# Optimization experiments

Measured on AMD Instinct MI355X. Metric: run time of the kernel, lower is better.

Reference implementation:

```python
import jax, jax.numpy as jnp
import numpy as np


def setup_inputs() -> dict:
    key = jax.random.key(0)
    k1, k2, k3 = jax.random.split(key, 3)
    N, C, W = 32, 64, 4096
    F, WW = 128, 64
    x = jax.random.normal(k1, (N, C, W), dtype=jnp.float32)
    w = jax.random.normal(k2, (F, C, WW), dtype=jnp.float32)
    b = jax.random.normal(k3, (F,), dtype=jnp.float32)
    return {"x": x, "w": w, "b": b}


def reference(x, w, b):
    # FFT-based 1D cross-correlation (the original loops over N, F, C; here batched).
    # x: [N, C, W], w: [F, C, WW], b: [F]
    N, C, W = x.shape
    F, _, WW = w.shape
    pad = 0  # module's padding kwarg
    fftsize = 1 << int(np.ceil(np.log2(W + 2 * pad + WW - 1)))  # next_power2
    out_W = W + 2 * pad - WW + 1
    # rfft of zero-padded signals and filters
    xfft = jnp.fft.rfft(x, n=fftsize, axis=-1)          # [N, C, K]
    wfft = jnp.fft.rfft(w, n=fftsize, axis=-1)          # [F, C, K]
    # cross-correlation: multiply by conj of filter spectrum, sum over channels
    offt = jnp.einsum('nck,fck->nfk', xfft, jnp.conj(wfft))  # [N, F, K]
    out = jnp.fft.irfft(offt, n=fftsize, axis=-1)[..., :out_W]  # real part, first out_W samples
    return out + b[None, :, None]
```

## Files before the change

### kernel.cpp

```cpp
#include <hip/hip_runtime.h>


#define C_TOT   64
#define F_TOT   128
#define KW      64
#define OUT_W   4033
#define W_IN    4096
#define N_BATCH 32
#define T_BLK   256
#define CH      2
#define XWIN    320
#define XSTR    384
#define TRS     260

typedef __attribute__((ext_vector_type(8))) short  short8;
typedef __attribute__((ext_vector_type(4))) float  floatx4;

union Frag { unsigned int u[4]; short8 v; };

__device__ inline unsigned short f32_to_bf16(float f) {
  unsigned int u = __float_as_uint(f);
  u += 0x7FFF + ((u >> 16) & 1);
  return (unsigned short)(u >> 16);
}

__device__ inline void async16(const unsigned short* g, unsigned short* l) {
  __builtin_amdgcn_global_load_lds(
      (const __attribute__((address_space(1))) unsigned int*)g,
      (__attribute__((address_space(3))) unsigned int*)l, 16, 0, 0);
}

__global__ __launch_bounds__(256) void conv1d_prep(
    const float* __restrict__ w, unsigned short* __restrict__ wsw) {
  int i4 = blockIdx.x * 256 + threadIdx.x;
  if (i4 < F_TOT * C_TOT * KW / 4) {
    int k4 = (i4 & 15) * 4;
    int c  = (i4 >> 4) & 63;
    int f  = i4 >> 10;
    float4 v = *(const float4*)&w[(size_t)i4 * 4];
    ushort4 o;
    o.x = f32_to_bf16(v.x); o.y = f32_to_bf16(v.y);
    o.z = f32_to_bf16(v.z); o.w = f32_to_bf16(v.w);
    int chunk = (k4 >> 3) ^ (f & 7);
    *(ushort4*)&wsw[((size_t)(c * F_TOT + f) * 8 + chunk) * 8 + (k4 & 7)] = o;
  }
}

__global__ __launch_bounds__(256, 2) void conv1d_mfma(
    const float* __restrict__ x, const unsigned short* __restrict__ wsw,
    const float* __restrict__ b, float* __restrict__ out) {
  __shared__ union SM {
    struct {
      unsigned short wls[2][CH * F_TOT * KW];
      unsigned short xls[2][CH * XSTR];
    } k;
    float tr[32 * TRS];
  } sm;

  const int tid  = threadIdx.x;
  const int lane = tid & 63;
  const int wv   = tid >> 6;
  const int q    = lane >> 4;
  const int col  = lane & 15;
  const int n    = blockIdx.y;
  const int t0   = blockIdx.x * T_BLK;
  const int fh2  = wv & 1;
  const int th   = wv >> 1;

  const int xc = tid / 80;
  const int xi = (tid - xc * 80) * 4;
  const float* xrowb = x + (size_t)n * C_TOT * W_IN;

  floatx4 acc[8][4];
#pragma unroll
  for (int ms = 0; ms < 8; ++ms)
#pragma unroll
    for (int ft = 0; ft < 4; ++ft) acc[ms][ft] = (floatx4)0.0f;

#define LOAD_X(cgx, vv)                                                         \
  {                                                                             \
    const float* src = xrowb + (size_t)((cgx) * CH + xc) * W_IN;                \
    int gt = t0 + xi;                                                           \
    if (gt + 3 < W_IN) vv = *(const float4*)(src + gt);                         \
    else {                                                                      \
      if (gt < W_IN)     vv.x = src[gt];                                        \
      if (gt + 1 < W_IN) vv.y = src[gt + 1];                                    \
      if (gt + 2 < W_IN) vv.z = src[gt + 2];                                    \
    }                                                                           \
  }

#define WRITE_X(p, vv)                                                          \
  {                                                                             \
    ushort4 o;                                                                  \
    o.x = f32_to_bf16(vv.x); o.y = f32_to_bf16(vv.y);                           \
    o.z = f32_to_bf16(vv.z); o.w = f32_to_bf16(vv.w);                           \
    *(ushort4*)&sm.k.xls[p][xc * XSTR + xi] = o;                                \
  }

#define STAGE_W(cg, p)                                                          \
  {                                                                             \
    const unsigned short* wbase = wsw + (size_t)(cg) * (CH * F_TOT * KW);       \
    _Pragma("unroll")                                                           \
    for (int s = 0; s < 8; ++s) {                                               \
      int off = (wv * 8 + s) * 512;                                             \
      async16(wbase + off + lane * 8, &sm.k.wls[p][off]);                       \
    }                                                                           \
  }

  if (tid < 160) {
    float4 xv = {0.f, 0.f, 0.f, 0.f};
    LOAD_X(0, xv)
    WRITE_X(0, xv)
  }
  STAGE_W(0, 0)
  __syncthreads();

  for (int cg = 0; cg < C_TOT / CH; ++cg) {
    const int p = cg & 1;
    const bool pre = (cg < C_TOT / CH - 1);
    float4 xv = {0.f, 0.f, 0.f, 0.f};
    if (pre && tid < 160) LOAD_X(cg + 1, xv)
    if (pre) STAGE_W(cg + 1, p ^ 1)

#pragma unroll
    for (int chl = 0; chl < CH; ++chl) {
      const unsigned short* xpb = &sm.k.xls[p][chl * XSTR];
      const unsigned short* wpb = &sm.k.wls[p][chl * F_TOT * KW];
#pragma unroll
      for (int h = 0; h < 2; ++h) {
        const int ab = 16 * col + 256 * th + 64 * h + 16 * q;
        const uint4 d0 = *(const uint4*)((const char*)xpb + ab);
        const uint4 d1 = *(const uint4*)((const char*)xpb + ab + 16);
        const unsigned int D[8] = {d0.x, d0.y, d0.z, d0.w, d1.x, d1.y, d1.z, d1.w};
        Frag A[8];
#pragma unroll
        for (int s = 0; s < 4; ++s)
#pragma unroll
          for (int i = 0; i < 4; ++i) {
            A[2 * s].u[i]     = D[s + i];
            A[2 * s + 1].u[i] = (D[s + i] >> 16) | (D[s + i + 1] << 16);
          }
        const int bs = ((h * 4 + q) ^ (col & 7)) * 8;
#pragma unroll
        for (int ft = 0; ft < 4; ++ft) {
          const short8 bf =
              *(const short8*)&wpb[(fh2 * 64 + ft * 16 + col) * KW + bs];
#pragma unroll
          for (int ms = 0; ms < 8; ++ms)
            acc[ms][ft] =
                __builtin_amdgcn_mfma_f32_16x16x32_bf16(A[ms].v, bf, acc[ms][ft], 0, 0, 0);
        }
      }
    }
    if (pre && tid < 160) WRITE_X(p ^ 1, xv)
    __syncthreads();
  }

  const int fs_w  = fh2 * 16 + col;
  const int fs_r  = tid >> 3;
  const int seg   = tid & 7;
  const int f_r   = (fs_r >> 4) * 64 + (fs_r & 15);
  const size_t ob = ((size_t)n * F_TOT) * OUT_W;

#pragma unroll
  for (int j = 0; j < 4; ++j) {
#pragma unroll
    for (int r = 0; r < 4; ++r)
#pragma unroll
      for (int g = 0; g < 2; ++g) {
        float4 vv;
        vv.x = acc[g * 4 + 0][j][r];
        vv.y = acc[g * 4 + 1][j][r];
        vv.z = acc[g * 4 + 2][j][r];
        vv.w = acc[g * 4 + 3][j][r];
        int tl = 32 * q + 8 * r + 4 * g + 128 * th;
        *(float4*)&sm.tr[fs_w * TRS + tl] = vv;
      }
    __syncthreads();
    const int f = f_r + 16 * j;
    const float bias = b[f];
    const size_t obf = ob + (size_t)f * OUT_W;
#pragma unroll
    for (int j2 = 0; j2 < 8; ++j2) {
      int tl = seg * 4 + 32 * j2;
      float4 vv = *(const float4*)&sm.tr[fs_r * TRS + tl];
      vv.x += bias; vv.y += bias; vv.z += bias; vv.w += bias;
      int t = t0 + tl;
      if (t + 3 < OUT_W) {
        *(float4*)&out[obf + t] = vv;
      } else {
        float e[4] = {vv.x, vv.y, vv.z, vv.w};
#pragma unroll
        for (int u = 0; u < 4; ++u)
          if (t + u < OUT_W) out[obf + t + u] = e[u];
      }
    }
    __syncthreads();
  }
}

extern "C" void kernel_launch(void* const* d_in, const int* in_sizes, int n_in,
                              void* d_out, int out_size, void* d_ws, size_t ws_size,
                              hipStream_t stream) {
  const float* x = (const float*)d_in[0];
  const float* w = (const float*)d_in[1];
  const float* b = (const float*)d_in[2];
  float* out = (float*)d_out;

  unsigned short* wsw = (unsigned short*)d_ws;

  conv1d_prep<<<(F_TOT * C_TOT * KW / 4 + 255) / 256, 256, 0, stream>>>(w, wsw);

  dim3 grid((OUT_W + T_BLK - 1) / T_BLK, N_BATCH);
  conv1d_mfma<<<grid, 256, 0, stream>>>(x, wsw, b, out);
}
```

Baseline: 186.2 us.

## Split filters across blocks to halve per-block tile and raise occupancy

Each block now computes 64 filters instead of 128, so the grid doubles to 32x32 blocks. This halves the accumulator registers and the weight LDS buffer, and launch bounds move to 4 blocks per SM. The MFMA inner loop is restructured to build A fragments per step rather than holding all eight. In exchange, each x tile is staged and converted twice, once for each filter half.

```diff
diff --git a/kernel.cpp b/kernel.cpp
--- a/kernel.cpp
+++ b/kernel.cpp
@@ -3,6 +3,7 @@
 
 #define C_TOT   64
 #define F_TOT   128
+#define F_BLK   64
 #define KW      64
 #define OUT_W   4033
 #define W_IN    4096
@@ -46,12 +47,12 @@
   }
 }
 
-__global__ __launch_bounds__(256, 2) void conv1d_mfma(
+__global__ __launch_bounds__(256, 4) void conv1d_mfma(
     const float* __restrict__ x, const unsigned short* __restrict__ wsw,
     const float* __restrict__ b, float* __restrict__ out) {
   __shared__ union SM {
     struct {
-      unsigned short wls[2][CH * F_TOT * KW];
+      unsigned short wls[2][CH * F_BLK * KW];
       unsigned short xls[2][CH * XSTR];
     } k;
     float tr[32 * TRS];
@@ -63,19 +64,21 @@
   const int q    = lane >> 4;
   const int col  = lane & 15;
   const int n    = blockIdx.y;
-  const int t0   = blockIdx.x * T_BLK;
-  const int fh2  = wv & 1;
+  const int bx   = blockIdx.x;
+  const int t0   = (bx & 15) * T_BLK;
+  const int FB   = (bx >> 4) * F_BLK;
+  const int fq   = wv & 1;
   const int th   = wv >> 1;
 
   const int xc = tid / 80;
   const int xi = (tid - xc * 80) * 4;
   const float* xrowb = x + (size_t)n * C_TOT * W_IN;
 
-  floatx4 acc[8][4];
+  floatx4 acc[8][2];
 #pragma unroll
   for (int ms = 0; ms < 8; ++ms)
 #pragma unroll
-    for (int ft = 0; ft < 4; ++ft) acc[ms][ft] = (floatx4)0.0f;
+    for (int ft = 0; ft < 2; ++ft) acc[ms][ft] = (floatx4)0.0f;
 
 #define LOAD_X(cgx, vv)                                                         \
   {                                                                             \
@@ -97,13 +100,15 @@
     *(ushort4*)&sm.k.xls[p][xc * XSTR + xi] = o;                                \
   }
 
-#define STAGE_W(cg, p)                                                          \
+#define STAGE_W(cg_, p_)                                                        \
   {                                                                             \
-    const unsigned short* wbase = wsw + (size_t)(cg) * (CH * F_TOT * KW);       \
+    const unsigned short* wb = wsw + ((size_t)(cg_) * CH * F_TOT + FB) * KW;    \
     _Pragma("unroll")                                                           \
-    for (int s = 0; s < 8; ++s) {                                               \
-      int off = (wv * 8 + s) * 512;                                             \
-      async16(wbase + off + lane * 8, &sm.k.wls[p][off]);                       \
+    for (int s = 0; s < 4; ++s) {                                               \
+      int off = (wv * 4 + s) * 512 + lane * 8;                                  \
+      int chl = off >> 12;                                                      \
+      int rem = off & 4095;                                                     \
+      async16(wb + (size_t)chl * F_TOT * KW + rem, &sm.k.wls[p_][off]);         \
     }                                                                           \
   }
 
@@ -125,30 +130,32 @@
 #pragma unroll
     for (int chl = 0; chl < CH; ++chl) {
       const unsigned short* xpb = &sm.k.xls[p][chl * XSTR];
-      const unsigned short* wpb = &sm.k.wls[p][chl * F_TOT * KW];
+      const unsigned short* wpb = &sm.k.wls[p][chl * F_BLK * KW];
 #pragma unroll
       for (int h = 0; h < 2; ++h) {
         const int ab = 16 * col + 256 * th + 64 * h + 16 * q;
         const uint4 d0 = *(const uint4*)((const char*)xpb + ab);
         const uint4 d1 = *(const uint4*)((const char*)xpb + ab + 16);
         const unsigned int D[8] = {d0.x, d0.y, d0.z, d0.w, d1.x, d1.y, d1.z, d1.w};
-        Frag A[8];
-#pragma unroll
-        for (int s = 0; s < 4; ++s)
+        const int bs = ((h * 4 + q) ^ (col & 7)) * 8;
+        const short8 bf0 = *(const short8*)&wpb[(fq * 32 + col) * KW + bs];
+        const short8 bf1 = *(const short8*)&wpb[(fq * 32 + 16 + col) * KW + bs];
+#pragma unroll
+        for (int s = 0; s < 4; ++s) {
+          Frag Ae, Ao;
 #pragma unroll
           for (int i = 0; i < 4; ++i) {
-            A[2 * s].u[i]     = D[s + i];
-            A[2 * s + 1].u[i] = (D[s + i] >> 16) | (D[s + i + 1] << 16);
+            Ae.u[i] = D[s + i];
+            Ao.u[i] = (D[s + i] >> 16) | (D[s + i + 1] << 16);
           }
-        const int bs = ((h * 4 + q) ^ (col & 7)) * 8;
-#pragma unroll
-        for (int ft = 0; ft < 4; ++ft) {
-          const short8 bf =
-              *(const short8*)&wpb[(fh2 * 64 + ft * 16 + col) * KW + bs];
-#pragma unroll
-          for (int ms = 0; ms < 8; ++ms)
-            acc[ms][ft] =
-                __builtin_amdgcn_mfma_f32_16x16x32_bf16(A[ms].v, bf, acc[ms][ft], 0, 0, 0);
+          acc[2 * s][0] =
+              __builtin_amdgcn_mfma_f32_16x16x32_bf16(Ae.v, bf0, acc[2 * s][0], 0, 0, 0);
+          acc[2 * s][1] =
+              __builtin_amdgcn_mfma_f32_16x16x32_bf16(Ae.v, bf1, acc[2 * s][1], 0, 0, 0);
+          acc[2 * s + 1][0] =
+              __builtin_amdgcn_mfma_f32_16x16x32_bf16(Ao.v, bf0, acc[2 * s + 1][0], 0, 0, 0);
+          acc[2 * s + 1][1] =
+              __builtin_amdgcn_mfma_f32_16x16x32_bf16(Ao.v, bf1, acc[2 * s + 1][1], 0, 0, 0);
         }
       }
     }
@@ -156,14 +163,13 @@
     __syncthreads();
   }
 
-  const int fs_w  = fh2 * 16 + col;
+  const int fs_w  = fq * 16 + col;
   const int fs_r  = tid >> 3;
   const int seg   = tid & 7;
-  const int f_r   = (fs_r >> 4) * 64 + (fs_r & 15);
   const size_t ob = ((size_t)n * F_TOT) * OUT_W;
 
 #pragma unroll
-  for (int j = 0; j < 4; ++j) {
+  for (int j = 0; j < 2; ++j) {
 #pragma unroll
     for (int r = 0; r < 4; ++r)
 #pragma unroll
@@ -177,7 +183,7 @@
         *(float4*)&sm.tr[fs_w * TRS + tl] = vv;
       }
     __syncthreads();
-    const int f = f_r + 16 * j;
+    const int f = FB + (fs_r >> 4) * 32 + j * 16 + (fs_r & 15);
     const float bias = b[f];
     const size_t obf = ob + (size_t)f * OUT_W;
 #pragma unroll
@@ -211,6 +217,6 @@
 
   conv1d_prep<<<(F_TOT * C_TOT * KW / 4 + 255) / 256, 256, 0, stream>>>(w, wsw);
 
-  dim3 grid((OUT_W + T_BLK - 1) / T_BLK, N_BATCH);
+  dim3 grid(32, N_BATCH);
   conv1d_mfma<<<grid, 256, 0, stream>>>(x, wsw, b, out);
 }
```

Result: slower. 225.5 us (+21.1%).

## Reorder conv GEMM reduction to iterate over taps with channel-major x tile

Applied to the files above, without the earlier changes.

The reduction loop changes from channel groups (reduce over the 64 filter taps inside each MFMA) to filter taps (reduce over channels inside each MFMA). The whole x window for all 64 channels is transposed into LDS once as bf16, and the weights are re-laid out per tap, so only a 16KB weight slice is streamed per step. This removes the register shuffling that built shifted A fragments and the per-iteration x loads. In exchange it adds a larger upfront x staging phase with scalar transposed LDS stores, and runs 64 barrier-synchronised iterations instead of 32.

```diff
diff --git a/kernel.cpp b/kernel.cpp
--- a/kernel.cpp
+++ b/kernel.cpp
@@ -8,15 +8,13 @@
 #define W_IN    4096
 #define N_BATCH 32
 #define T_BLK   256
-#define CH      2
-#define XWIN    320
-#define XSTR    384
+#define XROWS   320
+#define XSTR    72
 #define TRS     260
+#define BK_SH   8192
 
 typedef __attribute__((ext_vector_type(8))) short  short8;
 typedef __attribute__((ext_vector_type(4))) float  floatx4;
-
-union Frag { unsigned int u[4]; short8 v; };
 
 __device__ inline unsigned short f32_to_bf16(float f) {
   unsigned int u = __float_as_uint(f);
@@ -34,15 +32,17 @@
     const float* __restrict__ w, unsigned short* __restrict__ wsw) {
   int i4 = blockIdx.x * 256 + threadIdx.x;
   if (i4 < F_TOT * C_TOT * KW / 4) {
-    int k4 = (i4 & 15) * 4;
-    int c  = (i4 >> 4) & 63;
-    int f  = i4 >> 10;
-    float4 v = *(const float4*)&w[(size_t)i4 * 4];
+    int c4 = (i4 & 15) * 4;
+    int f  = (i4 >> 4) & 127;
+    int k  = i4 >> 11;
+    const float* src = w + ((size_t)f * C_TOT + c4) * KW + k;
     ushort4 o;
-    o.x = f32_to_bf16(v.x); o.y = f32_to_bf16(v.y);
-    o.z = f32_to_bf16(v.z); o.w = f32_to_bf16(v.w);
-    int chunk = (k4 >> 3) ^ (f & 7);
-    *(ushort4*)&wsw[((size_t)(c * F_TOT + f) * 8 + chunk) * 8 + (k4 & 7)] = o;
+    o.x = f32_to_bf16(src[0 * KW]);
+    o.y = f32_to_bf16(src[1 * KW]);
+    o.z = f32_to_bf16(src[2 * KW]);
+    o.w = f32_to_bf16(src[3 * KW]);
+    int chunk = (c4 >> 3) ^ (f & 7);
+    *(ushort4*)&wsw[((size_t)(k * F_TOT + f) * 8 + chunk) * 8 + (c4 & 7)] = o;
   }
 }
 
@@ -50,12 +50,10 @@
     const float* __restrict__ x, const unsigned short* __restrict__ wsw,
     const float* __restrict__ b, float* __restrict__ out) {
   __shared__ union SM {
-    struct {
-      unsigned short wls[2][CH * F_TOT * KW];
-      unsigned short xls[2][CH * XSTR];
-    } k;
+    unsigned short xt[XROWS * XSTR];
     float tr[32 * TRS];
   } sm;
+  __shared__ unsigned short bls[2][BK_SH];
 
   const int tid  = threadIdx.x;
   const int lane = tid & 63;
@@ -67,8 +65,6 @@
   const int fh2  = wv & 1;
   const int th   = wv >> 1;
 
-  const int xc = tid / 80;
-  const int xi = (tid - xc * 80) * 4;
   const float* xrowb = x + (size_t)n * C_TOT * W_IN;
 
   floatx4 acc[8][4];
@@ -77,82 +73,62 @@
 #pragma unroll
     for (int ft = 0; ft < 4; ++ft) acc[ms][ft] = (floatx4)0.0f;
 
-#define LOAD_X(cgx, vv)                                                         \
-  {                                                                             \
-    const float* src = xrowb + (size_t)((cgx) * CH + xc) * W_IN;                \
-    int gt = t0 + xi;                                                           \
-    if (gt + 3 < W_IN) vv = *(const float4*)(src + gt);                         \
-    else {                                                                      \
-      if (gt < W_IN)     vv.x = src[gt];                                        \
-      if (gt + 1 < W_IN) vv.y = src[gt + 1];                                    \
-      if (gt + 2 < W_IN) vv.z = src[gt + 2];                                    \
-    }                                                                           \
+#define STAGE_B(k_, p_)                                                        \
+  {                                                                            \
+    const unsigned short* wb = wsw + (size_t)(k_) * BK_SH;                     \
+    _Pragma("unroll")                                                          \
+    for (int s = 0; s < 4; ++s) {                                              \
+      int off = ((wv * 4 + s) * 64 + lane) * 8;                                \
+      async16(wb + off, &bls[p_][off]);                                        \
+    }                                                                          \
   }
 
-#define WRITE_X(p, vv)                                                          \
-  {                                                                             \
-    ushort4 o;                                                                  \
-    o.x = f32_to_bf16(vv.x); o.y = f32_to_bf16(vv.y);                           \
-    o.z = f32_to_bf16(vv.z); o.w = f32_to_bf16(vv.w);                           \
-    *(ushort4*)&sm.k.xls[p][xc * XSTR + xi] = o;                                \
+  STAGE_B(0, 0)
+#pragma unroll 4
+  for (int it = 0; it < 20; ++it) {
+    int j  = it * 256 + tid;
+    int c  = j / 80;
+    int tq = j - c * 80;
+    int gt = t0 + tq * 4;
+    const float* src = xrowb + (size_t)c * W_IN + gt;
+    float4 v = {0.f, 0.f, 0.f, 0.f};
+    if (gt + 3 < W_IN) v = *(const float4*)src;
+    else {
+      if (gt < W_IN)     v.x = src[0];
+      if (gt + 1 < W_IN) v.y = src[1];
+      if (gt + 2 < W_IN) v.z = src[2];
+    }
+    int rb = tq * 4;
+    sm.xt[(rb + 0) * XSTR + c] = f32_to_bf16(v.x);
+    sm.xt[(rb + 1) * XSTR + c] = f32_to_bf16(v.y);
+    sm.xt[(rb + 2) * XSTR + c] = f32_to_bf16(v.z);
+    sm.xt[(rb + 3) * XSTR + c] = f32_to_bf16(v.w);
   }
-
-#define STAGE_W(cg, p)                                                          \
-  {                                                                             \
-    const unsigned short* wbase = wsw + (size_t)(cg) * (CH * F_TOT * KW);       \
-    _Pragma("unroll")                                                           \
-    for (int s = 0; s < 8; ++s) {                                               \
-      int off = (wv * 8 + s) * 512;                                             \
-      async16(wbase + off + lane * 8, &sm.k.wls[p][off]);                       \
-    }                                                                           \
-  }
-
-  if (tid < 160) {
-    float4 xv = {0.f, 0.f, 0.f, 0.f};
-    LOAD_X(0, xv)
-    WRITE_X(0, xv)
-  }
-  STAGE_W(0, 0)
   __syncthreads();
 
-  for (int cg = 0; cg < C_TOT / CH; ++cg) {
-    const int p = cg & 1;
-    const bool pre = (cg < C_TOT / CH - 1);
-    float4 xv = {0.f, 0.f, 0.f, 0.f};
-    if (pre && tid < 160) LOAD_X(cg + 1, xv)
-    if (pre) STAGE_W(cg + 1, p ^ 1)
+#pragma unroll 2
+  for (int k = 0; k < KW; ++k) {
+    const int p = k & 1;
+    if (k + 1 < KW) STAGE_B(k + 1, p ^ 1)
+
+    const unsigned short* xk = &sm.xt[(th * 128 + col + k) * XSTR + q * 8];
+    const unsigned short* bp = &bls[p][(fh2 * 64 + col) * 64];
 
 #pragma unroll
-    for (int chl = 0; chl < CH; ++chl) {
-      const unsigned short* xpb = &sm.k.xls[p][chl * XSTR];
-      const unsigned short* wpb = &sm.k.wls[p][chl * F_TOT * KW];
+    for (int cstep = 0; cstep < 2; ++cstep) {
+      short8 Bf[4];
 #pragma unroll
-      for (int h = 0; h < 2; ++h) {
-        const int ab = 16 * col + 256 * th + 64 * h + 16 * q;
-        const uint4 d0 = *(const uint4*)((const char*)xpb + ab);
-        const uint4 d1 = *(const uint4*)((const char*)xpb + ab + 16);
-        const unsigned int D[8] = {d0.x, d0.y, d0.z, d0.w, d1.x, d1.y, d1.z, d1.w};
-        Frag A[8];
+      for (int ft = 0; ft < 4; ++ft)
+        Bf[ft] = *(const short8*)&bp[ft * 1024 + (((cstep << 2) + q) ^ (col & 7)) * 8];
 #pragma unroll
-        for (int s = 0; s < 4; ++s)
+      for (int ms = 0; ms < 8; ++ms) {
+        const short8 Af = *(const short8*)&xk[ms * 16 * XSTR + cstep * 32];
 #pragma unroll
-          for (int i = 0; i < 4; ++i) {
-            A[2 * s].u[i]     = D[s + i];
-            A[2 * s + 1].u[i] = (D[s + i] >> 16) | (D[s + i + 1] << 16);
-          }
-        const int bs = ((h * 4 + q) ^ (col & 7)) * 8;
-#pragma unroll
-        for (int ft = 0; ft < 4; ++ft) {
-          const short8 bf =
-              *(const short8*)&wpb[(fh2 * 64 + ft * 16 + col) * KW + bs];
-#pragma unroll
-          for (int ms = 0; ms < 8; ++ms)
-            acc[ms][ft] =
-                __builtin_amdgcn_mfma_f32_16x16x32_bf16(A[ms].v, bf, acc[ms][ft], 0, 0, 0);
-        }
+        for (int ft = 0; ft < 4; ++ft)
+          acc[ms][ft] =
+              __builtin_amdgcn_mfma_f32_16x16x32_bf16(Af, Bf[ft], acc[ms][ft], 0, 0, 0);
       }
     }
-    if (pre && tid < 160) WRITE_X(p ^ 1, xv)
     __syncthreads();
   }
 
@@ -165,17 +141,15 @@
 #pragma unroll
   for (int j = 0; j < 4; ++j) {
 #pragma unroll
-    for (int r = 0; r < 4; ++r)
-#pragma unroll
-      for (int g = 0; g < 2; ++g) {
-        float4 vv;
-        vv.x = acc[g * 4 + 0][j][r];
-        vv.y = acc[g * 4 + 1][j][r];
-        vv.z = acc[g * 4 + 2][j][r];
-        vv.w = acc[g * 4 + 3][j][r];
-        int tl = 32 * q + 8 * r + 4 * g + 128 * th;
-        *(float4*)&sm.tr[fs_w * TRS + tl] = vv;
-      }
+    for (int ms = 0; ms < 8; ++ms) {
+      float4 vv;
+      vv.x = acc[ms][j][0];
+      vv.y = acc[ms][j][1];
+      vv.z = acc[ms][j][2];
+      vv.w = acc[ms][j][3];
+      int tl = 128 * th + 16 * ms + 4 * q;
+      *(float4*)&sm.tr[fs_w * TRS + tl] = vv;
+    }
     __syncthreads();
     const int f = f_r + 16 * j;
     const float bias = b[f];
```

Result: slower. 197.5 us (+6.1%).
